# Optimization experiments

Measured on AMD Instinct MI355X. Metric: run time of the kernel, lower is better.

The kernel has to match this reference:

```python
import jax, jax.numpy as jnp
import numpy as np

ND, NG, E = 50000, 100000, 600000   # n_disease, n_gene, n_edges per direction
DIN, H, OUT = 128, 64, 64


def setup_inputs() -> dict:
    key = jax.random.key(0)
    ks = jax.random.split(key, 16)

    def w(k, i, o):
        return (jax.random.normal(k, (i, o), jnp.float32) / np.float32(np.sqrt(i)))

    return {
        "x_disease": jax.random.normal(ks[0], (ND, DIN), jnp.float32),
        "x_gene": jax.random.normal(ks[1], (NG, DIN), jnp.float32),
        "edge_src_dg": jax.random.randint(ks[2], (E,), 0, ND),
        "edge_dst_dg": jax.random.randint(ks[3], (E,), 0, NG),
        "edge_src_gd": jax.random.randint(ks[4], (E,), 0, NG),
        "edge_dst_gd": jax.random.randint(ks[5], (E,), 0, ND),
        "Wl1_dg": w(ks[6], DIN, H), "bl1_dg": jnp.zeros((H,), jnp.float32), "Wr1_dg": w(ks[7], DIN, H),
        "Wl1_gd": w(ks[8], DIN, H), "bl1_gd": jnp.zeros((H,), jnp.float32), "Wr1_gd": w(ks[9], DIN, H),
        "Wl2_dg": w(ks[10], H, OUT), "bl2_dg": jnp.zeros((OUT,), jnp.float32), "Wr2_dg": w(ks[11], H, OUT),
        "Wl2_gd": w(ks[12], H, OUT), "bl2_gd": jnp.zeros((OUT,), jnp.float32), "Wr2_gd": w(ks[13], H, OUT),
    }


def _sage(x_src, x_dst, src, dst, Wl, bl, Wr, n_dst):
    # SAGEConv (bipartite, aggr='mean'): lin_l(mean_j x_src[j]) + lin_r(x_dst)
    msg_sum = jax.ops.segment_sum(x_src[src], dst, num_segments=n_dst)   # [n_dst, d]
    cnt = jax.ops.segment_sum(jnp.ones((src.shape[0],), x_src.dtype), dst, num_segments=n_dst)
    mean = msg_sum / jnp.maximum(cnt, 1.0)[:, None]   # nodes w/o in-edges -> 0
    return mean @ Wl + bl + x_dst @ Wr


def reference(x_disease, x_gene, edge_src_dg, edge_dst_dg, edge_src_gd, edge_dst_gd,
              Wl1_dg, bl1_dg, Wr1_dg, Wl1_gd, bl1_gd, Wr1_gd,
              Wl2_dg, bl2_dg, Wr2_dg, Wl2_gd, bl2_gd, Wr2_gd):
    # layer 1: both relations read the original x_dict (HeteroConv semantics)
    g1 = _sage(x_disease, x_gene, edge_src_dg, edge_dst_dg, Wl1_dg, bl1_dg, Wr1_dg, NG)
    d1 = _sage(x_gene, x_disease, edge_src_gd, edge_dst_gd, Wl1_gd, bl1_gd, Wr1_gd, ND)
    # layer 2 (no nonlinearity in the original module)
    g2 = _sage(d1, g1, edge_src_dg, edge_dst_dg, Wl2_dg, bl2_dg, Wr2_dg, NG)
    d2 = _sage(g1, d1, edge_src_gd, edge_dst_gd, Wl2_gd, bl2_gd, Wr2_gd, ND)
    return d2, g2
```

## Files before the change

### kernel.cpp

```cpp
#include <hip/hip_runtime.h>

static constexpr int DIN = 128;
static constexpr int HID = 64;
static constexpr int BIN_SHIFT = 8;
static constexpr int CHUNK = 8192;

typedef short bf16x8 __attribute__((ext_vector_type(8)));
typedef float f32x4  __attribute__((ext_vector_type(4)));
typedef _Float16 half4 __attribute__((ext_vector_type(4)));
typedef _Float16 half8 __attribute__((ext_vector_type(8)));

__device__ __forceinline__ short f2bf(float f) {
    unsigned u = __float_as_uint(f);
    unsigned r = (u + 0x7fff + ((u >> 16) & 1)) >> 16;
    return (short)r;
}
__device__ __forceinline__ float bf2f(short s) {
    return __uint_as_float(((unsigned)(unsigned short)s) << 16);
}

__global__ __launch_bounds__(256) void binhist_kernel(
    const int* __restrict__ dstA, const int* __restrict__ dstB,
    int* __restrict__ binCnt, int nE, int gA, int nbA, int nbT)
{
    __shared__ int c[1024];
    for (int b = threadIdx.x; b < 1024; b += 256) c[b] = 0;
    __syncthreads();
    const int blk = blockIdx.x;
    const bool isA = blk < gA;
    const int* dst = isA ? dstA : dstB;
    const int off  = isA ? 0 : nbA;
    const int i0   = (isA ? blk : blk - gA) * CHUNK;
    #pragma unroll 4
    for (int k = 0; k < CHUNK / 256; ++k) {
        int i = i0 + k * 256 + threadIdx.x;
        if (i < nE) atomicAdd(&c[off + (dst[i] >> BIN_SHIFT)], 1);
    }
    __syncthreads();
    for (int b = threadIdx.x; b < nbT; b += 256) {
        int v = c[b];
        if (v) atomicAdd(&binCnt[b], v);
    }
}

__global__ __launch_bounds__(1024) void binscan_kernel(
    const int* __restrict__ binCnt, int* __restrict__ binBase,
    int* __restrict__ binCur, int nbT)
{
    __shared__ int s[1024];
    int v = (threadIdx.x < nbT) ? binCnt[threadIdx.x] : 0;
    s[threadIdx.x] = v;
    __syncthreads();
    for (int o = 1; o < 1024; o <<= 1) {
        int t = (threadIdx.x >= o) ? s[threadIdx.x - o] : 0;
        __syncthreads();
        s[threadIdx.x] += t;
        __syncthreads();
    }
    if (threadIdx.x < nbT) {
        binBase[threadIdx.x] = s[threadIdx.x] - v;
        binCur[threadIdx.x]  = s[threadIdx.x] - v;
    }
}

__global__ __launch_bounds__(256) void binplaceA_kernel(
    const int* __restrict__ srcA, const int* __restrict__ dstA,
    const int* __restrict__ srcB, const int* __restrict__ dstB,
    int* __restrict__ binCur, int2* __restrict__ pairs,
    int nE, int gA, int nbA, int nbT)
{
    __shared__ int cnt[1024];
    __shared__ int base[1024];
    for (int b = threadIdx.x; b < 1024; b += 256) cnt[b] = 0;
    __syncthreads();
    const int blk = blockIdx.x;
    const bool isA = blk < gA;
    const int* src = isA ? srcA : srcB;
    const int* dst = isA ? dstA : dstB;
    const int off  = isA ? 0 : nbA;
    const int i0   = (isA ? blk : blk - gA) * CHUNK;
    #pragma unroll 4
    for (int k = 0; k < CHUNK / 256; ++k) {
        int i = i0 + k * 256 + threadIdx.x;
        if (i < nE) atomicAdd(&cnt[off + (dst[i] >> BIN_SHIFT)], 1);
    }
    __syncthreads();
    for (int b = threadIdx.x; b < nbT; b += 256) {
        int v = cnt[b];
        base[b] = v ? atomicAdd(&binCur[b], v) : 0;
        cnt[b] = 0;
    }
    __syncthreads();
    #pragma unroll 4
    for (int k = 0; k < CHUNK / 256; ++k) {
        int i = i0 + k * 256 + threadIdx.x;
        if (i < nE) {
            int d  = dst[i];
            int bn = off + (d >> BIN_SHIFT);
            int p  = base[bn] + atomicAdd(&cnt[bn], 1);
            pairs[p] = make_int2(src[i], d);
        }
    }
}

__global__ __launch_bounds__(256) void binplaceB_kernel(
    const int2* __restrict__ pairs,
    const int* __restrict__ binBase, const int* __restrict__ binCnt,
    int* __restrict__ startsA, int* __restrict__ cntA, int* __restrict__ colA, int NA,
    int* __restrict__ startsB, int* __restrict__ cntB, int* __restrict__ colB, int NB,
    int nbA, int nE)
{
    __shared__ int lc[256];
    __shared__ int pr[256];
    const int b    = blockIdx.x;
    const bool isA = b < nbA;
    int* starts = isA ? startsA : startsB;
    int* cntN   = isA ? cntA : cntB;
    int* col    = isA ? colA : colB;
    const int N     = isA ? NA : NB;
    const int node0 = (isA ? b : b - nbA) << BIN_SHIFT;
    const int e0 = binBase[b];
    const int ec = binCnt[b];
    const int colBase = isA ? e0 : e0 - nE;

    lc[threadIdx.x] = 0;
    __syncthreads();
    for (int e = threadIdx.x; e < ec; e += 256)
        atomicAdd(&lc[pairs[e0 + e].y - node0], 1);
    __syncthreads();
    const int v = lc[threadIdx.x];
    pr[threadIdx.x] = v;
    __syncthreads();
    for (int o = 1; o < 256; o <<= 1) {
        int t = (threadIdx.x >= o) ? pr[threadIdx.x - o] : 0;
        __syncthreads();
        pr[threadIdx.x] += t;
        __syncthreads();
    }
    const int myStart = colBase + pr[threadIdx.x] - v;
    const int n = node0 + threadIdx.x;
    if (n < N) { starts[n] = myStart; cntN[n] = v; }
    __syncthreads();
    lc[threadIdx.x] = myStart;
    __syncthreads();
    for (int e = threadIdx.x; e < ec; e += 256) {
        int2 pd = pairs[e0 + e];
        int p = atomicAdd(&lc[pd.y - node0], 1);
        col[p] = pd.x;
    }
}

struct PackW {
    const float* Wa[4]; const float* Wb[4];
    short* oh[4]; short* ol[4];
    int K[4];
};

__global__ __launch_bounds__(256) void pack_w(PackW p) {
    const int c = blockIdx.y;
    const int K = p.K[c];
    const int t = blockIdx.x * 256 + threadIdx.x;
    if (t >= K * 16) return;
    const int f  = t >> 6, l = t & 63;
    const int ks = f >> 3, cf = f & 7;
    const int col = cf * 16 + (l & 15);
    const int kb  = ks * 32 + ((l >> 4) * 8);
    const float* s = (col < 64) ? (p.Wa[c] + col) : (p.Wb[c] + (col - 64));
    short* oh = p.oh[c] + (size_t)t * 8;
    short* ol = p.ol[c] + (size_t)t * 8;
    #pragma unroll
    for (int i = 0; i < 8; ++i) {
        float v = s[(kb + i) * 64];
        short h = f2bf(v);
        oh[i] = h;
        ol[i] = f2bf(v - bf2f(h));
    }
}

struct ProjJob {
    const float* x; const short* WH; const short* WL;
    _Float16* Pa; float* Pb; int N;
};

static constexpr int PA_LD = 72;
static constexpr int PB_LD = 68;

template<int K>
__global__ __launch_bounds__(256) void proj_mfma2(ProjJob a, ProjJob b, int blocksA)
{
    constexpr int NKS = K / 32;
    __shared__ short sWbuf[32768];
    short* sWH = sWbuf;
    short* sWL = sWbuf + K * 128;

    const bool isA = (int)blockIdx.x < blocksA;
    const ProjJob j = isA ? a : b;
    const int bid = isA ? blockIdx.x : blockIdx.x - blocksA;

    const int tid = threadIdx.x;
    const int l   = tid & 63;
    const int w   = tid >> 6;
    const int lr  = l & 15;
    const int lg  = l >> 4;
    const int r0  = bid * 64 + w * 16;
    const int row = r0 + lr;

    for (int t = tid; t < K * 16; t += 256) {
        *(bf16x8*)(sWH + t * 8) = *(const bf16x8*)(j.WH + t * 8);
        *(bf16x8*)(sWL + t * 8) = *(const bf16x8*)(j.WL + t * 8);
    }

    float4 u[NKS][2];
    {
        const bool ok = row < j.N;
        const float* xp = &j.x[(long long)row * K + lg * 8];
        #pragma unroll
        for (int ks = 0; ks < NKS; ++ks) {
            u[ks][0] = ok ? *(const float4*)(xp + ks * 32)     : make_float4(0.f,0.f,0.f,0.f);
            u[ks][1] = ok ? *(const float4*)(xp + ks * 32 + 4) : make_float4(0.f,0.f,0.f,0.f);
        }
    }
    __syncthreads();

    f32x4 acc[8];
    #pragma unroll
    for (int c = 0; c < 8; ++c) acc[c] = (f32x4){0.f, 0.f, 0.f, 0.f};

    #pragma unroll
    for (int ks = 0; ks < NKS; ++ks) {
        bf16x8 ah, al;
        {
            const float vv[8] = {u[ks][0].x, u[ks][0].y, u[ks][0].z, u[ks][0].w,
                                 u[ks][1].x, u[ks][1].y, u[ks][1].z, u[ks][1].w};
            #pragma unroll
            for (int i = 0; i < 8; ++i) {
                short h = f2bf(vv[i]);
                ah[i] = h;
                al[i] = f2bf(vv[i] - bf2f(h));
            }
        }
        const short* wb = sWH + (ks * 8) * 512 + l * 8;
        const short* lb = sWL + (ks * 8) * 512 + l * 8;
        #pragma unroll
        for (int cf = 0; cf < 8; ++cf) {
            const bf16x8 bh = *(const bf16x8*)(wb + cf * 512);
            const bf16x8 bl = *(const bf16x8*)(lb + cf * 512);
            acc[cf] = __builtin_amdgcn_mfma_f32_16x16x32_bf16(ah, bh, acc[cf], 0, 0, 0);
            acc[cf] = __builtin_amdgcn_mfma_f32_16x16x32_bf16(ah, bl, acc[cf], 0, 0, 0);
            acc[cf] = __builtin_amdgcn_mfma_f32_16x16x32_bf16(al, bh, acc[cf], 0, 0, 0);
        }
    }

    __syncthreads();
    _Float16* sPa = (_Float16*)sWbuf;
    float*    sPb = (float*)(sWbuf + 64 * PA_LD);

    #pragma unroll
    for (int q = 0; q < 4; ++q) {
        const int r = w * 16 + lg * 4 + q;
        #pragma unroll
        for (int cf = 0; cf < 8; ++cf) {
            const float v = acc[cf][q];
            if (cf < 4) sPa[r * PA_LD + cf * 16 + lr] = (_Float16)v;
            else        sPb[r * PB_LD + (cf - 4) * 16 + lr] = v;
        }
    }
    __syncthreads();

    for (int c = tid; c < 512; c += 256) {
        const int r = c >> 3, cc = (c & 7) * 8;
        const int gr = bid * 64 + r;
        if (gr < j.N)
            *(half8*)(j.Pa + (size_t)gr * 64 + cc) = *(half8*)(sPa + r * PA_LD + cc);
    }
    for (int c = tid; c < 1024; c += 256) {
        const int r = c >> 4, cc = (c & 15) * 4;
        const int gr = bid * 64 + r;
        if (gr < j.N)
            *(float4*)(j.Pb + (size_t)gr * 64 + cc) = *(float4*)(sPb + r * PB_LD + cc);
    }
}

struct GatherJob {
    const _Float16* P; const int* starts; const int* cnt; const int* col;
    const float* bias; float* out; int N;
};

__global__ __launch_bounds__(256) void gather2(GatherJob A, GatherJob B, int blocksA)
{
    const bool isA = (int)blockIdx.x < blocksA;
    const GatherJob g = isA ? A : B;
    const int bid = isA ? blockIdx.x : blockIdx.x - blocksA;

    const int lane = threadIdx.x & 63;
    const int wid  = (bid * 256 + threadIdx.x) >> 6;
    const int n    = wid * 4 + (lane >> 4);
    const int li   = lane & 15;
    if (n >= g.N) return;

    int e         = g.starts[n];
    const int deg = g.cnt[n];
    const int e1  = e + deg;

    float4 acc = make_float4(0.f, 0.f, 0.f, 0.f);
    while (e + 4 <= e1) {
        const int s0 = g.col[e], s1 = g.col[e + 1], s2 = g.col[e + 2], s3 = g.col[e + 3];
        const half4 v0 = *(const half4*)(g.P + (size_t)s0 * 64 + li * 4);
        const half4 v1 = *(const half4*)(g.P + (size_t)s1 * 64 + li * 4);
        const half4 v2 = *(const half4*)(g.P + (size_t)s2 * 64 + li * 4);
        const half4 v3 = *(const half4*)(g.P + (size_t)s3 * 64 + li * 4);
        acc.x += (float)v0[0] + (float)v1[0] + (float)v2[0] + (float)v3[0];
        acc.y += (float)v0[1] + (float)v1[1] + (float)v2[1] + (float)v3[1];
        acc.z += (float)v0[2] + (float)v1[2] + (float)v2[2] + (float)v3[2];
        acc.w += (float)v0[3] + (float)v1[3] + (float)v2[3] + (float)v3[3];
        e += 4;
    }
    while (e < e1) {
        const half4 v0 = *(const half4*)(g.P + (size_t)g.col[e] * 64 + li * 4);
        acc.x += (float)v0[0]; acc.y += (float)v0[1];
        acc.z += (float)v0[2]; acc.w += (float)v0[3];
        ++e;
    }
    const float inv = (deg > 0) ? 1.0f / (float)deg : 0.0f;
    const int c0 = li * 4;
    const float4 b4 = *(const float4*)&g.bias[c0];
    float4 cur = *(float4*)&g.out[(long long)n * 64 + c0];
    cur.x += acc.x * inv + b4.x;
    cur.y += acc.y * inv + b4.y;
    cur.z += acc.z * inv + b4.z;
    cur.w += acc.w * inv + b4.w;
    *(float4*)&g.out[(long long)n * 64 + c0] = cur;
}

extern "C" void kernel_launch(void* const* d_in, const int* in_sizes, int n_in,
                              void* d_out, int out_size, void* d_ws, size_t ws_size,
                              hipStream_t stream) {
    const float* x_d    = (const float*)d_in[0];
    const float* x_g    = (const float*)d_in[1];
    const int* src_dg   = (const int*)d_in[2];
    const int* dst_dg   = (const int*)d_in[3];
    const int* src_gd   = (const int*)d_in[4];
    const int* dst_gd   = (const int*)d_in[5];
    const float* Wl1_dg = (const float*)d_in[6];
    const float* bl1_dg = (const float*)d_in[7];
    const float* Wr1_dg = (const float*)d_in[8];
    const float* Wl1_gd = (const float*)d_in[9];
    const float* bl1_gd = (const float*)d_in[10];
    const float* Wr1_gd = (const float*)d_in[11];
    const float* Wl2_dg = (const float*)d_in[12];
    const float* bl2_dg = (const float*)d_in[13];
    const float* Wr2_dg = (const float*)d_in[14];
    const float* Wl2_gd = (const float*)d_in[15];
    const float* bl2_gd = (const float*)d_in[16];
    const float* Wr2_gd = (const float*)d_in[17];

    const int nd = in_sizes[0] / DIN;
    const int ng = in_sizes[1] / DIN;
    const int ne = in_sizes[2];

    _Float16* P_d = (_Float16*)d_ws;
    _Float16* P_g = P_d + (size_t)nd * HID;
    int* startsG = (int*)(P_g + (size_t)ng * HID);
    int* startsD = startsG + ng;
    int* cntG    = startsD + nd;
    int* cntD    = cntG + ng;
    int* colG    = cntD + nd;
    int* colD    = colG + ne;
    int* binCnt  = colD + ne;
    int* binBase = binCnt + 1024;
    int* binCur  = binBase + 1024;

    uintptr_t pp = (uintptr_t)(binCur + 1024);
    pp = (pp + 15) & ~(uintptr_t)15;
    int2* pairs = (int2*)pp;

    uintptr_t wp = (uintptr_t)(pairs + 2 * (size_t)ne);
    wp = (wp + 63) & ~(uintptr_t)63;
    short* wh0 = (short*)wp;
    short* wl0 = wh0 + 16384;
    short* wh1 = wl0 + 16384;
    short* wl1 = wh1 + 16384;
    short* wh2 = wl1 + 16384;
    short* wl2 = wh2 + 8192;
    short* wh3 = wl2 + 8192;
    short* wl3 = wh3 + 8192;

    float* out  = (float*)d_out;
    float* d1r  = out;
    float* g1r  = out + (size_t)nd * HID;

    const int gBH = (ne + CHUNK - 1) / CHUNK;
    const int nbG = (ng + 255) >> 8;
    const int nbD = (nd + 255) >> 8;
    const int nbT = nbG + nbD;
    const int gM_g = (ng + 63) / 64;
    const int gM_d = (nd + 63) / 64;
    const int gG_g = (ng + 15) / 16;
    const int gG_d = (nd + 15) / 16;

    PackW pw;
    pw.Wa[0] = Wl1_dg; pw.Wb[0] = Wr1_gd; pw.oh[0] = wh0; pw.ol[0] = wl0; pw.K[0] = 128;
    pw.Wa[1] = Wl1_gd; pw.Wb[1] = Wr1_dg; pw.oh[1] = wh1; pw.ol[1] = wl1; pw.K[1] = 128;
    pw.Wa[2] = Wl2_gd; pw.Wb[2] = Wr2_dg; pw.oh[2] = wh2; pw.ol[2] = wl2; pw.K[2] = 64;
    pw.Wa[3] = Wl2_dg; pw.Wb[3] = Wr2_gd; pw.oh[3] = wh3; pw.ol[3] = wl3; pw.K[3] = 64;
    pack_w<<<dim3(8, 4), 256, 0, stream>>>(pw);

    hipMemsetAsync(binCnt, 0, 1024 * sizeof(int), stream);

    binhist_kernel<<<2 * gBH, 256, 0, stream>>>(dst_dg, dst_gd, binCnt, ne, gBH, nbG, nbT);
    binscan_kernel<<<1, 1024, 0, stream>>>(binCnt, binBase, binCur, nbT);
    binplaceA_kernel<<<2 * gBH, 256, 0, stream>>>(src_dg, dst_dg, src_gd, dst_gd,
                                                  binCur, pairs, ne, gBH, nbG, nbT);
    binplaceB_kernel<<<nbT, 256, 0, stream>>>(pairs, binBase, binCnt,
                                              startsG, cntG, colG, ng,
                                              startsD, cntD, colD, nd, nbG, ne);

    ProjJob p1a = { x_d, wh0, wl0, P_d, d1r, nd };
    ProjJob p1b = { x_g, wh1, wl1, P_g, g1r, ng };
    proj_mfma2<DIN><<<gM_d + gM_g, 256, 0, stream>>>(p1a, p1b, gM_d);

    GatherJob ga1 = { P_d, startsG, cntG, colG, bl1_dg, g1r, ng };
    GatherJob gb1 = { P_g, startsD, cntD, colD, bl1_gd, d1r, nd };
    gather2<<<gG_g + gG_d, 256, 0, stream>>>(ga1, gb1, gG_g);

    ProjJob p2a = { g1r, wh2, wl2, P_g, g1r, ng };
    ProjJob p2b = { d1r, wh3, wl3, P_d, d1r, nd };
    proj_mfma2<HID><<<gM_g + gM_d, 256, 0, stream>>>(p2a, p2b, gM_g);

    GatherJob ga2 = { P_g, startsD, cntD, colD, bl2_gd, d1r, nd };
    GatherJob gb2 = { P_d, startsG, cntG, colG, bl2_dg, g1r, ng };
    gather2<<<gG_d + gG_g, 256, 0, stream>>>(ga2, gb2, gG_d);
}
```

Baseline: 327.1 us.

## Store layer-1 hidden states in fp16 and pack edge pairs into 32 bits

Layer-1 results (d1, g1) now live in fp16 workspace buffers instead of fp32 output arrays, which roughly halves traffic for the layer-1 gather read-modify-write and for the layer-2 projection input. Edge (src, dst) pairs in the binning sort are packed into one 32-bit word: the local dst offset goes in the top 8 bits and src in the low 24 bits. This halves pair-buffer traffic. The cost is fp16 rounding of the intermediate hidden features, plus the assumption that source node indices fit in 24 bits.

Result: faster. 316.9 us (-3.1%).

```diff
diff --git a/kernel.cpp b/kernel.cpp
--- a/kernel.cpp
+++ b/kernel.cpp
@@ -66,7 +66,7 @@
 __global__ __launch_bounds__(256) void binplaceA_kernel(
     const int* __restrict__ srcA, const int* __restrict__ dstA,
     const int* __restrict__ srcB, const int* __restrict__ dstB,
-    int* __restrict__ binCur, int2* __restrict__ pairs,
+    int* __restrict__ binCur, unsigned int* __restrict__ pairs,
     int nE, int gA, int nbA, int nbT)
 {
     __shared__ int cnt[1024];
@@ -98,13 +98,13 @@
             int d  = dst[i];
             int bn = off + (d >> BIN_SHIFT);
             int p  = base[bn] + atomicAdd(&cnt[bn], 1);
-            pairs[p] = make_int2(src[i], d);
+            pairs[p] = ((unsigned)(d & 255) << 24) | (unsigned)src[i];
         }
     }
 }
 
 __global__ __launch_bounds__(256) void binplaceB_kernel(
-    const int2* __restrict__ pairs,
+    const unsigned int* __restrict__ pairs,
     const int* __restrict__ binBase, const int* __restrict__ binCnt,
     int* __restrict__ startsA, int* __restrict__ cntA, int* __restrict__ colA, int NA,
     int* __restrict__ startsB, int* __restrict__ cntB, int* __restrict__ colB, int NB,
@@ -126,7 +126,7 @@
     lc[threadIdx.x] = 0;
     __syncthreads();
     for (int e = threadIdx.x; e < ec; e += 256)
-        atomicAdd(&lc[pairs[e0 + e].y - node0], 1);
+        atomicAdd(&lc[pairs[e0 + e] >> 24], 1);
     __syncthreads();
     const int v = lc[threadIdx.x];
     pr[threadIdx.x] = v;
@@ -144,9 +144,9 @@
     lc[threadIdx.x] = myStart;
     __syncthreads();
     for (int e = threadIdx.x; e < ec; e += 256) {
-        int2 pd = pairs[e0 + e];
-        int p = atomicAdd(&lc[pd.y - node0], 1);
-        col[p] = pd.x;
+        unsigned int pd = pairs[e0 + e];
+        int p = atomicAdd(&lc[pd >> 24], 1);
+        col[p] = (int)(pd & 0xFFFFFF);
     }
 }
 
@@ -177,24 +177,27 @@
     }
 }
 
-struct ProjJob {
-    const float* x; const short* WH; const short* WL;
-    _Float16* Pa; float* Pb; int N;
+template<typename TX, typename TB> struct ProjJobT {
+    const TX* x; const short* WH; const short* WL;
+    _Float16* Pa; TB* Pb; int N;
 };
 
 static constexpr int PA_LD = 72;
 static constexpr int PB_LD = 68;
 
-template<int K>
-__global__ __launch_bounds__(256) void proj_mfma2(ProjJob a, ProjJob b, int blocksA)
+template<int K, typename TX, typename TB>
+__global__ __launch_bounds__(256) void proj_mfma2(
+    ProjJobT<TX, TB> a, ProjJobT<TX, TB> b, int blocksA)
 {
     constexpr int NKS = K / 32;
-    __shared__ short sWbuf[32768];
+    constexpr int EPIL  = 4608 + (sizeof(TB) == 2 ? 4608 : 8704);
+    constexpr int LDSSH = (2 * K * 128 > EPIL) ? 2 * K * 128 : EPIL;
+    __shared__ short sWbuf[LDSSH];
     short* sWH = sWbuf;
     short* sWL = sWbuf + K * 128;
 
     const bool isA = (int)blockIdx.x < blocksA;
-    const ProjJob j = isA ? a : b;
+    const ProjJobT<TX, TB> j = isA ? a : b;
     const int bid = isA ? blockIdx.x : blockIdx.x - blocksA;
 
     const int tid = threadIdx.x;
@@ -210,14 +213,28 @@
         *(bf16x8*)(sWL + t * 8) = *(const bf16x8*)(j.WL + t * 8);
     }
 
-    float4 u[NKS][2];
+    float vv[NKS][8];
     {
         const bool ok = row < j.N;
-        const float* xp = &j.x[(long long)row * K + lg * 8];
         #pragma unroll
         for (int ks = 0; ks < NKS; ++ks) {
-            u[ks][0] = ok ? *(const float4*)(xp + ks * 32)     : make_float4(0.f,0.f,0.f,0.f);
-            u[ks][1] = ok ? *(const float4*)(xp + ks * 32 + 4) : make_float4(0.f,0.f,0.f,0.f);
+            if constexpr (sizeof(TX) == 4) {
+                const float* xp = (const float*)j.x + (long long)row * K + lg * 8;
+                float4 u0 = ok ? *(const float4*)(xp + ks * 32)     : make_float4(0.f,0.f,0.f,0.f);
+                float4 u1 = ok ? *(const float4*)(xp + ks * 32 + 4) : make_float4(0.f,0.f,0.f,0.f);
+                vv[ks][0]=u0.x; vv[ks][1]=u0.y; vv[ks][2]=u0.z; vv[ks][3]=u0.w;
+                vv[ks][4]=u1.x; vv[ks][5]=u1.y; vv[ks][6]=u1.z; vv[ks][7]=u1.w;
+            } else {
+                const _Float16* xp = (const _Float16*)j.x + (long long)row * K + lg * 8;
+                if (ok) {
+                    half8 h = *(const half8*)(xp + ks * 32);
+                    #pragma unroll
+                    for (int i = 0; i < 8; ++i) vv[ks][i] = (float)h[i];
+                } else {
+                    #pragma unroll
+                    for (int i = 0; i < 8; ++i) vv[ks][i] = 0.f;
+                }
+            }
         }
     }
     __syncthreads();
@@ -229,15 +246,11 @@
     #pragma unroll
     for (int ks = 0; ks < NKS; ++ks) {
         bf16x8 ah, al;
-        {
-            const float vv[8] = {u[ks][0].x, u[ks][0].y, u[ks][0].z, u[ks][0].w,
-                                 u[ks][1].x, u[ks][1].y, u[ks][1].z, u[ks][1].w};
-            #pragma unroll
-            for (int i = 0; i < 8; ++i) {
-                short h = f2bf(vv[i]);
-                ah[i] = h;
-                al[i] = f2bf(vv[i] - bf2f(h));
-            }
+        #pragma unroll
+        for (int i = 0; i < 8; ++i) {
+            short h = f2bf(vv[ks][i]);
+            ah[i] = h;
+            al[i] = f2bf(vv[ks][i] - bf2f(h));
         }
         const short* wb = sWH + (ks * 8) * 512 + l * 8;
         const short* lb = sWL + (ks * 8) * 512 + l * 8;
@@ -253,7 +266,8 @@
 
     __syncthreads();
     _Float16* sPa = (_Float16*)sWbuf;
-    float*    sPb = (float*)(sWbuf + 64 * PA_LD);
+    _Float16* sPbH = (_Float16*)(sWbuf + 64 * PA_LD);
+    float*    sPbF = (float*)(sWbuf + 64 * PA_LD);
 
     #pragma unroll
     for (int q = 0; q < 4; ++q) {
@@ -262,7 +276,10 @@
         for (int cf = 0; cf < 8; ++cf) {
             const float v = acc[cf][q];
             if (cf < 4) sPa[r * PA_LD + cf * 16 + lr] = (_Float16)v;
-            else        sPb[r * PB_LD + (cf - 4) * 16 + lr] = v;
+            else if constexpr (sizeof(TB) == 2)
+                sPbH[r * PA_LD + (cf - 4) * 16 + lr] = (_Float16)v;
+            else
+                sPbF[r * PB_LD + (cf - 4) * 16 + lr] = v;
         }
     }
     __syncthreads();
@@ -273,23 +290,36 @@
         if (gr < j.N)
             *(half8*)(j.Pa + (size_t)gr * 64 + cc) = *(half8*)(sPa + r * PA_LD + cc);
     }
-    for (int c = tid; c < 1024; c += 256) {
-        const int r = c >> 4, cc = (c & 15) * 4;
-        const int gr = bid * 64 + r;
-        if (gr < j.N)
-            *(float4*)(j.Pb + (size_t)gr * 64 + cc) = *(float4*)(sPb + r * PB_LD + cc);
-    }
-}
-
-struct GatherJob {
+    if constexpr (sizeof(TB) == 2) {
+        for (int c = tid; c < 512; c += 256) {
+            const int r = c >> 3, cc = (c & 7) * 8;
+            const int gr = bid * 64 + r;
+            if (gr < j.N)
+                *(half8*)((_Float16*)j.Pb + (size_t)gr * 64 + cc) =
+                    *(half8*)(sPbH + r * PA_LD + cc);
+        }
+    } else {
+        for (int c = tid; c < 1024; c += 256) {
+            const int r = c >> 4, cc = (c & 15) * 4;
+            const int gr = bid * 64 + r;
+            if (gr < j.N)
+                *(float4*)((float*)j.Pb + (size_t)gr * 64 + cc) =
+                    *(float4*)(sPbF + r * PB_LD + cc);
+        }
+    }
+}
+
+template<typename TO> struct GatherJobT {
     const _Float16* P; const int* starts; const int* cnt; const int* col;
-    const float* bias; float* out; int N;
+    const float* bias; TO* out; int N;
 };
 
-__global__ __launch_bounds__(256) void gather2(GatherJob A, GatherJob B, int blocksA)
+template<typename TO>
+__global__ __launch_bounds__(256) void gather2(
+    GatherJobT<TO> A, GatherJobT<TO> B, int blocksA)
 {
     const bool isA = (int)blockIdx.x < blocksA;
-    const GatherJob g = isA ? A : B;
+    const GatherJobT<TO> g = isA ? A : B;
     const int bid = isA ? blockIdx.x : blockIdx.x - blocksA;
 
     const int lane = threadIdx.x & 63;
@@ -324,12 +354,23 @@
     const float inv = (deg > 0) ? 1.0f / (float)deg : 0.0f;
     const int c0 = li * 4;
     const float4 b4 = *(const float4*)&g.bias[c0];
-    float4 cur = *(float4*)&g.out[(long long)n * 64 + c0];
-    cur.x += acc.x * inv + b4.x;
-    cur.y += acc.y * inv + b4.y;
-    cur.z += acc.z * inv + b4.z;
-    cur.w += acc.w * inv + b4.w;
-    *(float4*)&g.out[(long long)n * 64 + c0] = cur;
+    if constexpr (sizeof(TO) == 2) {
+        _Float16* op = (_Float16*)g.out + (size_t)n * 64 + c0;
+        half4 cur = *(half4*)op;
+        cur[0] = (_Float16)((float)cur[0] + acc.x * inv + b4.x);
+        cur[1] = (_Float16)((float)cur[1] + acc.y * inv + b4.y);
+        cur[2] = (_Float16)((float)cur[2] + acc.z * inv + b4.z);
+        cur[3] = (_Float16)((float)cur[3] + acc.w * inv + b4.w);
+        *(half4*)op = cur;
+    } else {
+        float* op = (float*)g.out + (size_t)n * 64 + c0;
+        float4 cur = *(float4*)op;
+        cur.x += acc.x * inv + b4.x;
+        cur.y += acc.y * inv + b4.y;
+        cur.z += acc.z * inv + b4.z;
+        cur.w += acc.w * inv + b4.w;
+        *(float4*)op = cur;
+    }
 }
 
 extern "C" void kernel_launch(void* const* d_in, const int* in_sizes, int n_in,
@@ -360,7 +401,9 @@
 
     _Float16* P_d = (_Float16*)d_ws;
     _Float16* P_g = P_d + (size_t)nd * HID;
-    int* startsG = (int*)(P_g + (size_t)ng * HID);
+    _Float16* d1h = P_g + (size_t)ng * HID;
+    _Float16* g1h = d1h + (size_t)nd * HID;
+    int* startsG = (int*)(g1h + (size_t)ng * HID);
     int* startsD = startsG + ng;
     int* cntG    = startsD + nd;
     int* cntD    = cntG + ng;
@@ -369,10 +412,7 @@
     int* binCnt  = colD + ne;
     int* binBase = binCnt + 1024;
     int* binCur  = binBase + 1024;
-
-    uintptr_t pp = (uintptr_t)(binCur + 1024);
-    pp = (pp + 15) & ~(uintptr_t)15;
-    int2* pairs = (int2*)pp;
+    unsigned int* pairs = (unsigned int*)(binCur + 1024);
 
     uintptr_t wp = (uintptr_t)(pairs + 2 * (size_t)ne);
     wp = (wp + 63) & ~(uintptr_t)63;
@@ -386,8 +426,8 @@
     short* wl3 = wh3 + 8192;
 
     float* out  = (float*)d_out;
-    float* d1r  = out;
-    float* g1r  = out + (size_t)nd * HID;
+    float* outD = out;
+    float* outG = out + (size_t)nd * HID;
 
     const int gBH = (ne + CHUNK - 1) / CHUNK;
     const int nbG = (ng + 255) >> 8;
@@ -415,19 +455,19 @@
                                               startsG, cntG, colG, ng,
                                               startsD, cntD, colD, nd, nbG, ne);
 
-    ProjJob p1a = { x_d, wh0, wl0, P_d, d1r, nd };
-    ProjJob p1b = { x_g, wh1, wl1, P_g, g1r, ng };
-    proj_mfma2<DIN><<<gM_d + gM_g, 256, 0, stream>>>(p1a, p1b, gM_d);
-
-    GatherJob ga1 = { P_d, startsG, cntG, colG, bl1_dg, g1r, ng };
-    GatherJob gb1 = { P_g, startsD, cntD, colD, bl1_gd, d1r, nd };
-    gather2<<<gG_g + gG_d, 256, 0, stream>>>(ga1, gb1, gG_g);
-
-    ProjJob p2a = { g1r, wh2, wl2, P_g, g1r, ng };
-    ProjJob p2b = { d1r, wh3, wl3, P_d, d1r, nd };
-    proj_mfma2<HID><<<gM_g + gM_d, 256, 0, stream>>>(p2a, p2b, gM_g);
-
-    GatherJob ga2 = { P_g, startsD, cntD, colD, bl2_gd, d1r, nd };
-    GatherJob gb2 = { P_d, startsG, cntG, colG, bl2_dg, g1r, ng };
-    gather2<<<gG_d + gG_g, 256, 0, stream>>>(ga2, gb2, gG_d);
-}
+    ProjJobT<float, _Float16> p1a = { x_d, wh0, wl0, P_d, d1h, nd };
+    ProjJobT<float, _Float16> p1b = { x_g, wh1, wl1, P_g, g1h, ng };
+    proj_mfma2<DIN, float, _Float16><<<gM_d + gM_g, 256, 0, stream>>>(p1a, p1b, gM_d);
+
+    GatherJobT<_Float16> ga1 = { P_d, startsG, cntG, colG, bl1_dg, g1h, ng };
+    GatherJobT<_Float16> gb1 = { P_g, startsD, cntD, colD, bl1_gd, d1h, nd };
+    gather2<_Float16><<<gG_g + gG_d, 256, 0, stream>>>(ga1, gb1, gG_g);
+
+    ProjJobT<_Float16, float> p2a = { g1h, wh2, wl2, P_g, outG, ng };
+    ProjJobT<_Float16, float> p2b = { d1h, wh3, wl3, P_d, outD, nd };
+    proj_mfma2<HID, _Float16, float><<<gM_g + gM_d, 256, 0, stream>>>(p2a, p2b, gM_g);
+
+    GatherJobT<float> ga2 = { P_g, startsD, cntD, colD, bl2_gd, outD, nd };
+    GatherJobT<float> gb2 = { P_d, startsG, cntG, colG, bl2_dg, outG, ng };
+    gather2<float><<<gG_d + gG_g, 256, 0, stream>>>(ga2, gb2, gG_d);
+}
```
